# Performance work log

Hardware: AMD Instinct MI355X
Metric: run time of the kernel (lower is better)

## Reference

```python
import jax, jax.numpy as jnp
import numpy as np

B, S, D = 4, 2048, 1024


def setup_inputs() -> dict:
    key = jax.random.key(0)
    ks = jax.random.split(key, 8)
    x = jax.random.normal(ks[0], (B, S, D), dtype=jnp.float32)
    # additive causal mask: 0 on/below diagonal, -1e9 above
    causal = jnp.tril(jnp.ones((S, S), dtype=bool))
    mask = jnp.where(causal, 0.0, -1e9).astype(jnp.float32)[None, :, :]  # [1,S,S]
    scale = 1.0 / np.sqrt(D)
    Wq = jax.random.normal(ks[1], (D, D), dtype=jnp.float32) * scale
    bq = jnp.zeros((D,), dtype=jnp.float32)
    Wk = jax.random.normal(ks[2], (D, D), dtype=jnp.float32) * scale
    bk = jnp.zeros((D,), dtype=jnp.float32)
    Wv = jax.random.normal(ks[3], (D, D), dtype=jnp.float32) * scale
    bv = jnp.zeros((D,), dtype=jnp.float32)
    return {"x": x, "mask": mask, "Wq": Wq, "bq": bq, "Wk": Wk, "bk": bk, "Wv": Wv, "bv": bv}


def reference(x, mask, Wq, bq, Wk, bk, Wv, bv):
    # Q/K/V projections (torch Linear: y = x @ W^T + b)
    q = jnp.einsum('bsd,ed->bse', x, Wq) + bq
    k = jnp.einsum('bsd,ed->bse', x, Wk) + bk
    v = jnp.einsum('bsd,ed->bse', x, Wv) + bv
    d = x.shape[-1]
    scores = jnp.einsum('bqd,bkd->bqk', q, k) / jnp.sqrt(jnp.float32(d))
    scores = scores + mask
    attn = jax.nn.softmax(scores, axis=-1)
    return jnp.einsum('bqk,bkd->bqd', attn, v)
```

## Files before the change

### kernel.cpp

```cpp
#include <hip/hip_runtime.h>
#include <hip/hip_bf16.h>


typedef __attribute__((ext_vector_type(8))) short short8;
typedef __attribute__((ext_vector_type(4))) float f32x4;
typedef __attribute__((ext_vector_type(4))) unsigned short ushort4v;

static __device__ __forceinline__ unsigned short f2b(float f) {
  union { __hip_bfloat16 h; unsigned short u; } cv;
  cv.h = __float2bfloat16(f);
  return cv.u;
}

#define GLOAD_LDS16(gsrc, ldst)                                              \
  __builtin_amdgcn_global_load_lds(                                          \
      (const __attribute__((address_space(1))) void*)(gsrc),                 \
      (__attribute__((address_space(3))) void*)(ldst), 16, 0, 0)

#define WAIT_VM0() asm volatile("s_waitcnt vmcnt(0)" ::: "memory")

__global__ __launch_bounds__(256) void cvt4(const float* __restrict__ in,
                                            unsigned short* __restrict__ out, int n4) {
  int i = blockIdx.x * blockDim.x + threadIdx.x;
  if (i >= n4) return;
  float4 v = reinterpret_cast<const float4*>(in)[i];
  ushort4v o;
  o.x = f2b(v.x); o.y = f2b(v.y); o.z = f2b(v.z); o.w = f2b(v.w);
  reinterpret_cast<ushort4v*>(out)[i] = o;
}

__global__ __launch_bounds__(256) void prep_w(
    const float* __restrict__ Wq, const float* __restrict__ Wk, const float* __restrict__ Wv,
    const float* __restrict__ bq, const float* __restrict__ bk, const float* __restrict__ bv,
    unsigned short* __restrict__ Wb, float* __restrict__ biasb) {
  int id = blockIdx.x;
  if (id < 3072) {
    int sel = id >> 10;
    const float* src = sel == 0 ? Wq : sel == 1 ? Wk : Wv;
    int i = (id & 1023) * 256 + threadIdx.x;
    float4 v = reinterpret_cast<const float4*>(src)[i];
    ushort4v o;
    o.x = f2b(v.x); o.y = f2b(v.y); o.z = f2b(v.z); o.w = f2b(v.w);
    reinterpret_cast<ushort4v*>(Wb + (long)sel * 1048576)[i] = o;
  } else {
    int i = (id - 3072) * 256 + threadIdx.x;
    if (i < 3072) {
      int sel = i >> 10;
      const float* src = sel == 0 ? bq : sel == 1 ? bk : bv;
      biasb[i] = src[i & 1023];
    }
  }
}

__global__ __launch_bounds__(256) void proj_gemm(
    const unsigned short* __restrict__ A, const unsigned short* __restrict__ B,
    unsigned short* __restrict__ Cout, const float* __restrict__ bias,
    int lda, int ldb, int ldc, int ktiles) {
  int bx = blockIdx.x, by = blockIdx.y;

  __shared__ unsigned short sA[128 * 64];
  __shared__ unsigned short sB[128 * 64];

  int tid = threadIdx.x;
  int lane = tid & 63;
  int w = tid >> 6;
  int wr = w >> 1, wc = w & 1;

  const unsigned short* Ab = A + (long)by * 128 * lda;
  const unsigned short* Bb = B + (long)bx * 128 * ldb;

  f32x4 acc[4][4];
#pragma unroll
  for (int m = 0; m < 4; ++m)
#pragma unroll
    for (int n = 0; n < 4; ++n) acc[m][n] = (f32x4){0.f, 0.f, 0.f, 0.f};

  for (int kt = 0; kt < ktiles; ++kt) {
    __syncthreads();
#pragma unroll
    for (int c = 0; c < 8; ++c) {
      int chunk = w * 8 + c;
      int half = chunk & 15;
      int L = half * 1024 + lane * 16;
      int row = L >> 7;
      int gs = ((L >> 4) & 7) ^ (row & 7);
      if (chunk < 16) {
        GLOAD_LDS16(Ab + (long)row * lda + kt * 64 + gs * 8, sA + half * 512);
      } else {
        GLOAD_LDS16(Bb + (long)row * ldb + kt * 64 + gs * 8, sB + half * 512);
      }
    }
    __syncthreads();

#pragma unroll
    for (int kk = 0; kk < 2; ++kk) {
      short8 af[4], bfr[4];
#pragma unroll
      for (int m = 0; m < 4; ++m) {
        int row = wr * 64 + m * 16 + (lane & 15);
        int g = kk * 4 + (lane >> 4);
        af[m] = *(const short8*)((const char*)sA + row * 128 + ((g ^ (row & 7)) << 4));
      }
#pragma unroll
      for (int n = 0; n < 4; ++n) {
        int row = wc * 64 + n * 16 + (lane & 15);
        int g = kk * 4 + (lane >> 4);
        bfr[n] = *(const short8*)((const char*)sB + row * 128 + ((g ^ (row & 7)) << 4));
      }
#pragma unroll
      for (int m = 0; m < 4; ++m)
#pragma unroll
        for (int n = 0; n < 4; ++n)
          acc[m][n] = __builtin_amdgcn_mfma_f32_16x16x32_bf16(af[m], bfr[n], acc[m][n], 0, 0, 0);
    }
  }

  int r0 = by * 128 + wr * 64 + (lane >> 4) * 4;
  int c0 = bx * 128 + wc * 64 + (lane & 15);
#pragma unroll
  for (int m = 0; m < 4; ++m)
#pragma unroll
    for (int n = 0; n < 4; ++n) {
      int gc = c0 + n * 16;
      float bv = bias[gc];
#pragma unroll
      for (int r = 0; r < 4; ++r)
        Cout[(long)(r0 + m * 16 + r) * ldc + gc] = f2b(acc[m][n][r] + bv);
    }
}

__global__ __launch_bounds__(256) void scores_gemm(
    const unsigned short* __restrict__ QKV, float* __restrict__ S) {
  __shared__ unsigned short sA[2][128 * 64];
  __shared__ unsigned short sB[2][128 * 64];
  int c8 = blockIdx.x, j = blockIdx.y;
  int by = (j <= c8) ? c8 : 15 - c8;
  int bx = (j <= c8) ? j : j - c8 - 1;
  long bz = blockIdx.z;
  const unsigned short* Q = QKV + bz * (2048L * 3072);
  const unsigned short* Ab = Q + (long)by * 128 * 3072;
  const unsigned short* Bb = Q + 1024 + (long)bx * 128 * 3072;

  int tid = threadIdx.x;
  int lane = tid & 63;
  int w = tid >> 6;
  int wr = w >> 1, wc = w & 1;

  f32x4 acc[4][4];
#pragma unroll
  for (int m = 0; m < 4; ++m)
#pragma unroll
    for (int n = 0; n < 4; ++n) acc[m][n] = (f32x4){0.f, 0.f, 0.f, 0.f};

#define SC_STAGE(BUF, KT)                                                        \
  do {                                                                           \
    _Pragma("unroll") for (int c = 0; c < 8; ++c) {                              \
      int chunk = w * 8 + c;                                                     \
      int half = chunk & 15;                                                     \
      int L = half * 1024 + lane * 16;                                           \
      int row = L >> 7;                                                          \
      int gs = ((L >> 4) & 7) ^ (row & 7);                                       \
      if (chunk < 16) {                                                          \
        GLOAD_LDS16(Ab + (long)row * 3072 + (KT) * 64 + gs * 8,                  \
                    &sA[BUF][half * 512]);                                       \
      } else {                                                                   \
        GLOAD_LDS16(Bb + (long)row * 3072 + (KT) * 64 + gs * 8,                  \
                    &sB[BUF][half * 512]);                                       \
      }                                                                          \
    }                                                                            \
  } while (0)

#define SC_COMPUTE(BUF)                                                          \
  do {                                                                           \
    _Pragma("unroll") for (int kk = 0; kk < 2; ++kk) {                           \
      short8 af[4], bfr[4];                                                      \
      _Pragma("unroll") for (int m = 0; m < 4; ++m) {                            \
        int row = wr * 64 + m * 16 + (lane & 15);                                \
        int g = kk * 4 + (lane >> 4);                                            \
        af[m] = *(const short8*)((const char*)sA[BUF] + row * 128 +              \
                                 ((g ^ (row & 7)) << 4));                        \
      }                                                                          \
      _Pragma("unroll") for (int n = 0; n < 4; ++n) {                            \
        int row = wc * 64 + n * 16 + (lane & 15);                                \
        int g = kk * 4 + (lane >> 4);                                            \
        bfr[n] = *(const short8*)((const char*)sB[BUF] + row * 128 +             \
                                  ((g ^ (row & 7)) << 4));                       \
      }                                                                          \
      _Pragma("unroll") for (int m = 0; m < 4; ++m)                              \
          _Pragma("unroll") for (int n = 0; n < 4; ++n) acc[m][n] =              \
          __builtin_amdgcn_mfma_f32_16x16x32_bf16(af[m], bfr[n], acc[m][n],      \
                                                  0, 0, 0);                      \
    }                                                                            \
  } while (0)

  SC_STAGE(0, 0);
  WAIT_VM0();
  __builtin_amdgcn_s_barrier();
#pragma unroll 1
  for (int kt = 0; kt < 16; kt += 2) {
    if (kt + 1 < 16) SC_STAGE(1, kt + 1);
    SC_COMPUTE(0);
    WAIT_VM0();
    __builtin_amdgcn_s_barrier();
    if (kt + 2 < 16) SC_STAGE(0, kt + 2);
    SC_COMPUTE(1);
    WAIT_VM0();
    __builtin_amdgcn_s_barrier();
  }

  float* Sb = S + bz * (2048L * 2048);
  int r0 = by * 128 + wr * 64 + (lane >> 4) * 4;
  int c0 = bx * 128 + wc * 64 + (lane & 15);
#pragma unroll
  for (int m = 0; m < 4; ++m)
#pragma unroll
    for (int n = 0; n < 4; ++n)
#pragma unroll
      for (int r = 0; r < 4; ++r)
        Sb[(long)(r0 + m * 16 + r) * 2048 + c0 + n * 16] = acc[m][n][r] * 0.03125f;
#undef SC_STAGE
#undef SC_COMPUTE
}

__global__ __launch_bounds__(256) void transpose64(const unsigned short* __restrict__ V,
                                                   unsigned short* __restrict__ Vt) {
  __shared__ unsigned short t[64][72];
  int s0 = blockIdx.x * 64, d0 = blockIdx.y * 64;
  long bz = blockIdx.z;
  const unsigned short* src = V + bz * (2048L * 3072);
  unsigned short* dst = Vt + bz * (1024L * 2048);
  int tid = threadIdx.x;
#pragma unroll
  for (int pp = 0; pp < 2; ++pp) {
    int r = pp * 32 + (tid >> 3);
    int c = (tid & 7) * 8;
    short8 v = *(const short8*)(src + (long)(s0 + r) * 3072 + d0 + c);
    *(short8*)&t[r][c] = v;
  }
  __syncthreads();
#pragma unroll
  for (int pp = 0; pp < 2; ++pp) {
    int d = pp * 32 + (tid >> 3);
    int sc = (tid & 7) * 8;
    short8 v;
#pragma unroll
    for (int k = 0; k < 8; ++k) v[k] = (short)t[sc + k][d];
    *(short8*)(dst + (long)(d0 + d) * 2048 + s0 + sc) = v;
  }
}

__global__ __launch_bounds__(64) void softmax_causal(float* __restrict__ S) {
  int row = blockIdx.x;
  long b = row >> 11;
  int i = row & 2047;
  float* s = S + (b * 2048 + i) * 2048;
  unsigned short* p = (unsigned short*)s;
  int n = i + 1;
  int jEnd = ((i >> 7) + 1) << 7;
  int lane = threadIdx.x;

  float vals[32];
  float m = -3.0e38f;
#pragma unroll
  for (int k = 0; k < 32; ++k) {
    int j = lane + k * 64;
    vals[k] = (j < n) ? s[j] : -3.0e38f;
    m = fmaxf(m, vals[k]);
  }
#pragma unroll
  for (int off = 32; off > 0; off >>= 1) m = fmaxf(m, __shfl_xor(m, off));

  float sum = 0.f;
#pragma unroll
  for (int k = 0; k < 32; ++k) {
    int j = lane + k * 64;
    float e = (j < n) ? __expf(vals[k] - m) : 0.f;
    vals[k] = e;
    sum += e;
  }
#pragma unroll
  for (int off = 32; off > 0; off >>= 1) sum += __shfl_xor(sum, off);
  float inv = 1.0f / sum;
#pragma unroll
  for (int k = 0; k < 32; ++k) {
    int j = lane + k * 64;
    if (j < jEnd) p[j] = f2b(vals[k] * inv);
  }
}

__global__ __launch_bounds__(512) void pv_gemm(
    const unsigned short* __restrict__ P, const unsigned short* __restrict__ Vt,
    float* __restrict__ out) {
  __shared__ unsigned short sA[2][128 * 64];
  __shared__ unsigned short sB[2][128 * 64];
  int tid = threadIdx.x;
  int lane = tid & 63;
  int w = tid >> 6;
  int wr = w >> 2, wc = w & 3;
  int byp = blockIdx.x, bx = blockIdx.y, bz = blockIdx.z;
  const unsigned short* Pb = P + bz * (2048L * 4096);
  const unsigned short* Bb = Vt + bz * (1024L * 2048) + (long)bx * 128 * 2048;
  float* Ob = out + bz * (2048L * 1024);

#define PV_STAGE(BUF, KT)                                                        \
  do {                                                                           \
    _Pragma("unroll") for (int c = 0; c < 4; ++c) {                              \
      int chunk = w * 4 + c;                                                     \
      int hh = chunk & 15;                                                       \
      int L = hh * 1024 + lane * 16;                                             \
      int row = L >> 7;                                                          \
      int gs = ((L >> 4) & 7) ^ (row & 7);                                       \
      if (chunk < 16) {                                                          \
        GLOAD_LDS16(Ab + (long)row * 4096 + (KT) * 64 + gs * 8,                  \
                    &sA[BUF][hh * 512]);                                         \
      } else {                                                                   \
        GLOAD_LDS16(Bb + (long)row * 2048 + (KT) * 64 + gs * 8,                  \
                    &sB[BUF][hh * 512]);                                         \
      }                                                                          \
    }                                                                            \
  } while (0)

#define PV_COMPUTE(BUF)                                                          \
  do {                                                                           \
    _Pragma("unroll") for (int kk = 0; kk < 2; ++kk) {                           \
      short8 af[4], bf2[2];                                                      \
      _Pragma("unroll") for (int m = 0; m < 4; ++m) {                            \
        int row = wr * 64 + m * 16 + (lane & 15);                                \
        int g = kk * 4 + (lane >> 4);                                            \
        af[m] = *(const short8*)((const char*)sA[BUF] + row * 128 +              \
                                 ((g ^ (row & 7)) << 4));                        \
      }                                                                          \
      _Pragma("unroll") for (int n = 0; n < 2; ++n) {                            \
        int row = wc * 32 + n * 16 + (lane & 15);                                \
        int g = kk * 4 + (lane >> 4);                                            \
        bf2[n] = *(const short8*)((const char*)sB[BUF] + row * 128 +             \
                                  ((g ^ (row & 7)) << 4));                       \
      }                                                                          \
      _Pragma("unroll") for (int m = 0; m < 4; ++m)                              \
          _Pragma("unroll") for (int n = 0; n < 2; ++n) acc[m][n] =              \
          __builtin_amdgcn_mfma_f32_16x16x32_bf16(af[m], bf2[n], acc[m][n],      \
                                                  0, 0, 0);                      \
    }                                                                            \
  } while (0)

#pragma unroll 1
  for (int half = 0; half < 2; ++half) {
    int strip = half == 0 ? (15 - byp) : byp;
    int nkt = (strip + 1) * 2;
    const unsigned short* Ab = Pb + (long)strip * 128 * 4096;

    f32x4 acc[4][2];
#pragma unroll
    for (int m = 0; m < 4; ++m)
#pragma unroll
      for (int n = 0; n < 2; ++n) acc[m][n] = (f32x4){0.f, 0.f, 0.f, 0.f};

    PV_STAGE(0, 0);
    WAIT_VM0();
    __builtin_amdgcn_s_barrier();
#pragma unroll 1
    for (int kt = 0; kt < nkt; kt += 2) {
      PV_STAGE(1, kt + 1);
      PV_COMPUTE(0);
      WAIT_VM0();
      __builtin_amdgcn_s_barrier();
      if (kt + 2 < nkt) PV_STAGE(0, kt + 2);
      PV_COMPUTE(1);
      WAIT_VM0();
      __builtin_amdgcn_s_barrier();
    }

    int r0 = strip * 128 + wr * 64 + (lane >> 4) * 4;
    int c0 = bx * 128 + wc * 32 + (lane & 15);
#pragma unroll
    for (int m = 0; m < 4; ++m)
#pragma unroll
      for (int n = 0; n < 2; ++n)
#pragma unroll
        for (int r = 0; r < 4; ++r)
          Ob[(long)(r0 + m * 16 + r) * 1024 + c0 + n * 16] = acc[m][n][r];
  }
#undef PV_STAGE
#undef PV_COMPUTE
}

extern "C" void kernel_launch(void* const* d_in, const int* in_sizes, int n_in,
                              void* d_out, int out_size, void* d_ws, size_t ws_size,
                              hipStream_t stream) {
  const float* x = (const float*)d_in[0];
  const float* Wq = (const float*)d_in[2];
  const float* bq = (const float*)d_in[3];
  const float* Wk = (const float*)d_in[4];
  const float* bk = (const float*)d_in[5];
  const float* Wv = (const float*)d_in[6];
  const float* bv = (const float*)d_in[7];
  float* out = (float*)d_out;

  char* ws = (char*)d_ws;
  const long MB = 1 << 20;
  unsigned short* xb = (unsigned short*)(ws);
  unsigned short* Wb = (unsigned short*)(ws + 16 * MB);
  float* biasb = (float*)(ws + 22 * MB);
  unsigned short* QKV = (unsigned short*)(ws + 23 * MB);
  unsigned short* Vt = (unsigned short*)(ws + 71 * MB);
  float* Sbuf = (float*)(ws + 87 * MB);

  cvt4<<<8192, 256, 0, stream>>>(x, xb, 2097152);
  prep_w<<<3084, 256, 0, stream>>>(Wq, Wk, Wv, bq, bk, bv, Wb, biasb);

  proj_gemm<<<dim3(24, 64), 256, 0, stream>>>(xb, Wb, QKV, biasb, 1024, 1024, 3072, 16);

  transpose64<<<dim3(32, 16, 4), 256, 0, stream>>>(QKV + 2048, Vt);

  scores_gemm<<<dim3(8, 17, 4), 256, 0, stream>>>(QKV, Sbuf);

  softmax_causal<<<8192, 64, 0, stream>>>(Sbuf);

  pv_gemm<<<dim3(8, 8, 4), 512, 0, stream>>>((unsigned short*)Sbuf, Vt, out);
}
```

Before: 267.3 us.

## Fuse V transpose into projection epilogue, store scores as bf16, merge prep kernels

Merges the x and weight conversion kernels into a single prep launch. The projection GEMM now writes V already transposed through an LDS tile in its epilogue, which removes the separate transpose kernel. Scores are written as bf16 instead of fp32, and softmax reads and writes paired bf16 values in place. This halves score-buffer traffic and drops two launches, but rounding the logits to bf16 before softmax loses precision.

```diff
diff --git a/kernel.cpp b/kernel.cpp
--- a/kernel.cpp
+++ b/kernel.cpp
@@ -5,12 +5,18 @@
 typedef __attribute__((ext_vector_type(8))) short short8;
 typedef __attribute__((ext_vector_type(4))) float f32x4;
 typedef __attribute__((ext_vector_type(4))) unsigned short ushort4v;
+typedef __attribute__((ext_vector_type(2))) unsigned short ushort2v;
 
 static __device__ __forceinline__ unsigned short f2b(float f) {
   union { __hip_bfloat16 h; unsigned short u; } cv;
   cv.h = __float2bfloat16(f);
   return cv.u;
 }
+static __device__ __forceinline__ float b2f(unsigned short u) {
+  union { unsigned int i; float f; } cv;
+  cv.i = ((unsigned int)u) << 16;
+  return cv.f;
+}
 
 #define GLOAD_LDS16(gsrc, ldst)                                              \
   __builtin_amdgcn_global_load_lds(                                          \
@@ -19,31 +25,30 @@
 
 #define WAIT_VM0() asm volatile("s_waitcnt vmcnt(0)" ::: "memory")
 
-__global__ __launch_bounds__(256) void cvt4(const float* __restrict__ in,
-                                            unsigned short* __restrict__ out, int n4) {
-  int i = blockIdx.x * blockDim.x + threadIdx.x;
-  if (i >= n4) return;
-  float4 v = reinterpret_cast<const float4*>(in)[i];
-  ushort4v o;
-  o.x = f2b(v.x); o.y = f2b(v.y); o.z = f2b(v.z); o.w = f2b(v.w);
-  reinterpret_cast<ushort4v*>(out)[i] = o;
-}
-
-__global__ __launch_bounds__(256) void prep_w(
+__global__ __launch_bounds__(256) void prep(
+    const float* __restrict__ x,
     const float* __restrict__ Wq, const float* __restrict__ Wk, const float* __restrict__ Wv,
     const float* __restrict__ bq, const float* __restrict__ bk, const float* __restrict__ bv,
-    unsigned short* __restrict__ Wb, float* __restrict__ biasb) {
+    unsigned short* __restrict__ xb, unsigned short* __restrict__ Wb,
+    float* __restrict__ biasb) {
   int id = blockIdx.x;
-  if (id < 3072) {
-    int sel = id >> 10;
+  if (id < 8192) {
+    int i = id * 256 + threadIdx.x;
+    float4 v = reinterpret_cast<const float4*>(x)[i];
+    ushort4v o;
+    o.x = f2b(v.x); o.y = f2b(v.y); o.z = f2b(v.z); o.w = f2b(v.w);
+    reinterpret_cast<ushort4v*>(xb)[i] = o;
+  } else if (id < 11264) {
+    int id2 = id - 8192;
+    int sel = id2 >> 10;
     const float* src = sel == 0 ? Wq : sel == 1 ? Wk : Wv;
-    int i = (id & 1023) * 256 + threadIdx.x;
+    int i = (id2 & 1023) * 256 + threadIdx.x;
     float4 v = reinterpret_cast<const float4*>(src)[i];
     ushort4v o;
     o.x = f2b(v.x); o.y = f2b(v.y); o.z = f2b(v.z); o.w = f2b(v.w);
     reinterpret_cast<ushort4v*>(Wb + (long)sel * 1048576)[i] = o;
   } else {
-    int i = (id - 3072) * 256 + threadIdx.x;
+    int i = (id - 11264) * 256 + threadIdx.x;
     if (i < 3072) {
       int sel = i >> 10;
       const float* src = sel == 0 ? bq : sel == 1 ? bk : bv;
@@ -54,20 +59,21 @@
 
 __global__ __launch_bounds__(256) void proj_gemm(
     const unsigned short* __restrict__ A, const unsigned short* __restrict__ B,
-    unsigned short* __restrict__ Cout, const float* __restrict__ bias,
-    int lda, int ldb, int ldc, int ktiles) {
+    unsigned short* __restrict__ QKout, unsigned short* __restrict__ VtOut,
+    const float* __restrict__ bias) {
   int bx = blockIdx.x, by = blockIdx.y;
 
-  __shared__ unsigned short sA[128 * 64];
-  __shared__ unsigned short sB[128 * 64];
+  __shared__ unsigned short sbuf[2 * 128 * 64];
+  unsigned short* sA = sbuf;
+  unsigned short* sB = sbuf + 128 * 64;
 
   int tid = threadIdx.x;
   int lane = tid & 63;
   int w = tid >> 6;
   int wr = w >> 1, wc = w & 1;
 
-  const unsigned short* Ab = A + (long)by * 128 * lda;
-  const unsigned short* Bb = B + (long)bx * 128 * ldb;
+  const unsigned short* Ab = A + (long)by * 128 * 1024;
+  const unsigned short* Bb = B + (long)bx * 128 * 1024;
 
   f32x4 acc[4][4];
 #pragma unroll
@@ -75,7 +81,7 @@
 #pragma unroll
     for (int n = 0; n < 4; ++n) acc[m][n] = (f32x4){0.f, 0.f, 0.f, 0.f};
 
-  for (int kt = 0; kt < ktiles; ++kt) {
+  for (int kt = 0; kt < 16; ++kt) {
     __syncthreads();
 #pragma unroll
     for (int c = 0; c < 8; ++c) {
@@ -85,9 +91,9 @@
       int row = L >> 7;
       int gs = ((L >> 4) & 7) ^ (row & 7);
       if (chunk < 16) {
-        GLOAD_LDS16(Ab + (long)row * lda + kt * 64 + gs * 8, sA + half * 512);
+        GLOAD_LDS16(Ab + (long)row * 1024 + kt * 64 + gs * 8, sA + half * 512);
       } else {
-        GLOAD_LDS16(Bb + (long)row * ldb + kt * 64 + gs * 8, sB + half * 512);
+        GLOAD_LDS16(Bb + (long)row * 1024 + kt * 64 + gs * 8, sB + half * 512);
       }
     }
     __syncthreads();
@@ -115,31 +121,67 @@
     }
   }
 
-  int r0 = by * 128 + wr * 64 + (lane >> 4) * 4;
-  int c0 = bx * 128 + wc * 64 + (lane & 15);
-#pragma unroll
-  for (int m = 0; m < 4; ++m)
-#pragma unroll
-    for (int n = 0; n < 4; ++n) {
-      int gc = c0 + n * 16;
-      float bv = bias[gc];
-#pragma unroll
-      for (int r = 0; r < 4; ++r)
-        Cout[(long)(r0 + m * 16 + r) * ldc + gc] = f2b(acc[m][n][r] + bv);
-    }
+  if (bx < 16) {
+    int r0 = by * 128 + wr * 64 + (lane >> 4) * 4;
+    int c0 = bx * 128 + wc * 64 + (lane & 15);
+#pragma unroll
+    for (int m = 0; m < 4; ++m)
+#pragma unroll
+      for (int n = 0; n < 4; ++n) {
+        int gc = c0 + n * 16;
+        float bv = bias[gc];
+#pragma unroll
+        for (int r = 0; r < 4; ++r)
+          QKout[(long)(r0 + m * 16 + r) * 2048 + gc] = f2b(acc[m][n][r] + bv);
+      }
+  } else {
+    __syncthreads();
+    unsigned short(*T)[132] = (unsigned short(*)[132])sbuf;
+    int sl0 = wr * 64 + (lane >> 4) * 4;
+    int d0 = (bx - 16) * 128;
+    long b = by >> 4;
+    int s0 = (by & 15) * 128;
+    unsigned short* VT = VtOut + b * (1024L * 2048) + (long)d0 * 2048 + s0;
+#pragma unroll
+    for (int h = 0; h < 2; ++h) {
+      if (wc == h) {
+#pragma unroll
+        for (int m = 0; m < 4; ++m)
+#pragma unroll
+          for (int n = 0; n < 4; ++n) {
+            int dloc = (lane & 15) + n * 16;
+            float bv = bias[2048 + d0 + h * 64 + dloc];
+            ushort4v o;
+            o.x = f2b(acc[m][n][0] + bv);
+            o.y = f2b(acc[m][n][1] + bv);
+            o.z = f2b(acc[m][n][2] + bv);
+            o.w = f2b(acc[m][n][3] + bv);
+            *(ushort4v*)&T[dloc][sl0 + m * 16] = o;
+          }
+      }
+      __syncthreads();
+#pragma unroll
+      for (int pass = 0; pass < 8; ++pass) {
+        int d = pass * 8 + (tid >> 5);
+        int c = (tid & 31) * 4;
+        ushort4v v = *(const ushort4v*)&T[d][c];
+        *(ushort4v*)(VT + (long)(h * 64 + d) * 2048 + c) = v;
+      }
+      __syncthreads();
+    }
+  }
 }
 
 __global__ __launch_bounds__(256) void scores_gemm(
-    const unsigned short* __restrict__ QKV, float* __restrict__ S) {
+    const unsigned short* __restrict__ QK, unsigned short* __restrict__ S) {
   __shared__ unsigned short sA[2][128 * 64];
   __shared__ unsigned short sB[2][128 * 64];
   int c8 = blockIdx.x, j = blockIdx.y;
   int by = (j <= c8) ? c8 : 15 - c8;
   int bx = (j <= c8) ? j : j - c8 - 1;
   long bz = blockIdx.z;
-  const unsigned short* Q = QKV + bz * (2048L * 3072);
-  const unsigned short* Ab = Q + (long)by * 128 * 3072;
-  const unsigned short* Bb = Q + 1024 + (long)bx * 128 * 3072;
+  const unsigned short* Ab = QK + (bz * 2048 + (long)by * 128) * 2048;
+  const unsigned short* Bb = QK + (bz * 2048 + (long)bx * 128) * 2048 + 1024;
 
   int tid = threadIdx.x;
   int lane = tid & 63;
@@ -161,10 +203,10 @@
       int row = L >> 7;                                                          \
       int gs = ((L >> 4) & 7) ^ (row & 7);                                       \
       if (chunk < 16) {                                                          \
-        GLOAD_LDS16(Ab + (long)row * 3072 + (KT) * 64 + gs * 8,                  \
+        GLOAD_LDS16(Ab + (long)row * 2048 + (KT) * 64 + gs * 8,                  \
                     &sA[BUF][half * 512]);                                       \
       } else {                                                                   \
-        GLOAD_LDS16(Bb + (long)row * 3072 + (KT) * 64 + gs * 8,                  \
+        GLOAD_LDS16(Bb + (long)row * 2048 + (KT) * 64 + gs * 8,                  \
                     &sB[BUF][half * 512]);                                       \
       }                                                                          \
     }                                                                            \
@@ -208,7 +250,7 @@
     __builtin_amdgcn_s_barrier();
   }
 
-  float* Sb = S + bz * (2048L * 2048);
+  unsigned short* Sb = S + bz * (2048L * 2048);
   int r0 = by * 128 + wr * 64 + (lane >> 4) * 4;
   int c0 = bx * 128 + wc * 64 + (lane & 15);
 #pragma unroll
@@ -217,44 +259,16 @@
     for (int n = 0; n < 4; ++n)
 #pragma unroll
       for (int r = 0; r < 4; ++r)
-        Sb[(long)(r0 + m * 16 + r) * 2048 + c0 + n * 16] = acc[m][n][r] * 0.03125f;
+        Sb[(long)(r0 + m * 16 + r) * 2048 + c0 + n * 16] = f2b(acc[m][n][r] * 0.03125f);
 #undef SC_STAGE
 #undef SC_COMPUTE
 }
 
-__global__ __launch_bounds__(256) void transpose64(const unsigned short* __restrict__ V,
-                                                   unsigned short* __restrict__ Vt) {
-  __shared__ unsigned short t[64][72];
-  int s0 = blockIdx.x * 64, d0 = blockIdx.y * 64;
-  long bz = blockIdx.z;
-  const unsigned short* src = V + bz * (2048L * 3072);
-  unsigned short* dst = Vt + bz * (1024L * 2048);
-  int tid = threadIdx.x;
-#pragma unroll
-  for (int pp = 0; pp < 2; ++pp) {
-    int r = pp * 32 + (tid >> 3);
-    int c = (tid & 7) * 8;
-    short8 v = *(const short8*)(src + (long)(s0 + r) * 3072 + d0 + c);
-    *(short8*)&t[r][c] = v;
-  }
-  __syncthreads();
-#pragma unroll
-  for (int pp = 0; pp < 2; ++pp) {
-    int d = pp * 32 + (tid >> 3);
-    int sc = (tid & 7) * 8;
-    short8 v;
-#pragma unroll
-    for (int k = 0; k < 8; ++k) v[k] = (short)t[sc + k][d];
-    *(short8*)(dst + (long)(d0 + d) * 2048 + s0 + sc) = v;
-  }
-}
-
-__global__ __launch_bounds__(64) void softmax_causal(float* __restrict__ S) {
+__global__ __launch_bounds__(64) void softmax_causal(unsigned short* __restrict__ S) {
   int row = blockIdx.x;
   long b = row >> 11;
   int i = row & 2047;
-  float* s = S + (b * 2048 + i) * 2048;
-  unsigned short* p = (unsigned short*)s;
+  unsigned short* s = S + (b * 2048 + i) * 2048;
   int n = i + 1;
   int jEnd = ((i >> 7) + 1) << 7;
   int lane = threadIdx.x;
@@ -262,18 +276,22 @@
   float vals[32];
   float m = -3.0e38f;
 #pragma unroll
+  for (int k = 0; k < 16; ++k) {
+    int j0 = lane * 2 + k * 128;
+    ushort2v v = *(const ushort2v*)(s + j0);
+    float a = (j0 < n) ? b2f(v.x) : -3.0e38f;
+    float bb = (j0 + 1 < n) ? b2f(v.y) : -3.0e38f;
+    vals[2 * k] = a;
+    vals[2 * k + 1] = bb;
+    m = fmaxf(m, fmaxf(a, bb));
+  }
+#pragma unroll
+  for (int off = 32; off > 0; off >>= 1) m = fmaxf(m, __shfl_xor(m, off));
+
+  float sum = 0.f;
+#pragma unroll
   for (int k = 0; k < 32; ++k) {
-    int j = lane + k * 64;
-    vals[k] = (j < n) ? s[j] : -3.0e38f;
-    m = fmaxf(m, vals[k]);
-  }
-#pragma unroll
-  for (int off = 32; off > 0; off >>= 1) m = fmaxf(m, __shfl_xor(m, off));
-
-  float sum = 0.f;
-#pragma unroll
-  for (int k = 0; k < 32; ++k) {
-    int j = lane + k * 64;
+    int j = (lane * 2) + (k >> 1) * 128 + (k & 1);
     float e = (j < n) ? __expf(vals[k] - m) : 0.f;
     vals[k] = e;
     sum += e;
@@ -282,9 +300,14 @@
   for (int off = 32; off > 0; off >>= 1) sum += __shfl_xor(sum, off);
   float inv = 1.0f / sum;
 #pragma unroll
-  for (int k = 0; k < 32; ++k) {
-    int j = lane + k * 64;
-    if (j < jEnd) p[j] = f2b(vals[k] * inv);
+  for (int k = 0; k < 16; ++k) {
+    int j0 = lane * 2 + k * 128;
+    if (j0 < jEnd) {
+      ushort2v o;
+      o.x = f2b(vals[2 * k] * inv);
+      o.y = f2b(vals[2 * k + 1] * inv);
+      *(ushort2v*)(s + j0) = o;
+    }
   }
 }
 
@@ -298,7 +321,7 @@
   int w = tid >> 6;
   int wr = w >> 2, wc = w & 3;
   int byp = blockIdx.x, bx = blockIdx.y, bz = blockIdx.z;
-  const unsigned short* Pb = P + bz * (2048L * 4096);
+  const unsigned short* Pb = P + bz * (2048L * 2048);
   const unsigned short* Bb = Vt + bz * (1024L * 2048) + (long)bx * 128 * 2048;
   float* Ob = out + bz * (2048L * 1024);
 
@@ -311,7 +334,7 @@
       int row = L >> 7;                                                          \
       int gs = ((L >> 4) & 7) ^ (row & 7);                                       \
       if (chunk < 16) {                                                          \
-        GLOAD_LDS16(Ab + (long)row * 4096 + (KT) * 64 + gs * 8,                  \
+        GLOAD_LDS16(Ab + (long)row * 2048 + (KT) * 64 + gs * 8,                  \
                     &sA[BUF][hh * 512]);                                         \
       } else {                                                                   \
         GLOAD_LDS16(Bb + (long)row * 2048 + (KT) * 64 + gs * 8,                  \
@@ -347,7 +370,7 @@
   for (int half = 0; half < 2; ++half) {
     int strip = half == 0 ? (15 - byp) : byp;
     int nkt = (strip + 1) * 2;
-    const unsigned short* Ab = Pb + (long)strip * 128 * 4096;
+    const unsigned short* Ab = Pb + (long)strip * 128 * 2048;
 
     f32x4 acc[4][2];
 #pragma unroll
@@ -401,20 +424,17 @@
   unsigned short* xb = (unsigned short*)(ws);
   unsigned short* Wb = (unsigned short*)(ws + 16 * MB);
   float* biasb = (float*)(ws + 22 * MB);
-  unsigned short* QKV = (unsigned short*)(ws + 23 * MB);
-  unsigned short* Vt = (unsigned short*)(ws + 71 * MB);
-  float* Sbuf = (float*)(ws + 87 * MB);
-
-  cvt4<<<8192, 256, 0, stream>>>(x, xb, 2097152);
-  prep_w<<<3084, 256, 0, stream>>>(Wq, Wk, Wv, bq, bk, bv, Wb, biasb);
-
-  proj_gemm<<<dim3(24, 64), 256, 0, stream>>>(xb, Wb, QKV, biasb, 1024, 1024, 3072, 16);
-
-  transpose64<<<dim3(32, 16, 4), 256, 0, stream>>>(QKV + 2048, Vt);
-
-  scores_gemm<<<dim3(8, 17, 4), 256, 0, stream>>>(QKV, Sbuf);
+  unsigned short* QK = (unsigned short*)(ws + 23 * MB);
+  unsigned short* Vt = (unsigned short*)(ws + 55 * MB);
+  unsigned short* Sbuf = (unsigned short*)(ws + 71 * MB);
+
+  prep<<<11276, 256, 0, stream>>>(x, Wq, Wk, Wv, bq, bk, bv, xb, Wb, biasb);
+
+  proj_gemm<<<dim3(24, 64), 256, 0, stream>>>(xb, Wb, QK, Vt, biasb);
+
+  scores_gemm<<<dim3(8, 17, 4), 256, 0, stream>>>(QK, Sbuf);
 
   softmax_causal<<<8192, 64, 0, stream>>>(Sbuf);
 
-  pv_gemm<<<dim3(8, 8, 4), 512, 0, stream>>>((unsigned short*)Sbuf, Vt, out);
-}
+  pv_gemm<<<dim3(8, 8, 4), 512, 0, stream>>>(Sbuf, Vt, out);
+}
```

Result: faster. 258.5 us (-3.3%).
